# Performance work log

Hardware: AMD Instinct MI355X
Metric: run time of the kernel (lower is better)

Reference implementation:

```python
import jax, jax.numpy as jnp
import numpy as np


def setup_inputs() -> dict:
    key = jax.random.key(0)
    k1, k2, k3, k4 = jax.random.split(key, 4)
    in_features, out_features = 4096, 11008
    n_tokens = 64
    x = jax.random.normal(k1, (n_tokens, in_features), dtype=jnp.float32)
    # int8-valued weights stored as int32 (values in [-128, 127] range subset)
    weight_int = jax.random.randint(k2, (out_features, in_features), 0, 127, dtype=jnp.int32)
    weight_scale = jnp.float32(0.01)
    weight_zero_point = 3  # scalar int zero point
    bias = jax.random.normal(k3, (out_features,), dtype=jnp.float32) * 0.02
    return {
        "x": x,
        "weight_int": weight_int,
        "weight_scale": weight_scale,
        "weight_zero_point": weight_zero_point,
        "bias": bias,
    }


def reference(x, weight_int, weight_scale, weight_zero_point, bias):
    # Dequantize: W = (W_int - zp) * scale, shape [out, in]
    w = (weight_int.astype(jnp.float32) - jnp.float32(weight_zero_point)) * weight_scale
    # F.linear: y = x @ W^T + b
    out = jnp.einsum("ti,oi->to", x, w)
    return out + bias
```

## Files before the change

### kernel.cpp

```cpp
#include <hip/hip_runtime.h>
#include <hip/hip_bf16.h>

typedef __attribute__((ext_vector_type(8))) short short8;
typedef __attribute__((ext_vector_type(4))) float f32x4;
typedef __attribute__((ext_vector_type(4))) int   int4v;

#define IN_F  4096
#define OUT_F 11008
#define NTOK  64
#define BK    64
#define NIT   (IN_F / BK)
#define DEPTH 4

__device__ __forceinline__ short bf16_rne(float f) {
    unsigned u = __builtin_bit_cast(unsigned, f);
    u += 0x7FFFu + ((u >> 16) & 1u);
    return (short)(u >> 16);
}

__device__ __forceinline__ void gld16(const void* g, void* l) {
    __builtin_amdgcn_global_load_lds(
        (const __attribute__((address_space(1))) unsigned int*)g,
        (__attribute__((address_space(3))) unsigned int*)l,
        16, 0, 0);
}

__global__ __launch_bounds__(256)
void xcast(const float* __restrict__ x, unsigned short* __restrict__ xb) {
    const int i = (blockIdx.x * 256 + threadIdx.x) * 8;
    f32x4 a = *(const f32x4*)(x + i);
    f32x4 b = *(const f32x4*)(x + i + 4);
    short8 o;
#pragma unroll
    for (int j = 0; j < 4; ++j) { o[j] = bf16_rne(a[j]); o[j + 4] = bf16_rne(b[j]); }
    *(short8*)(xb + i) = o;
}

#define STAGE(IT) do {                                                        \
    const int _s = (IT) & (DEPTH - 1);                                        \
    gld16(wsrc + (size_t)(IT) * BK,             (char*)wt[_s] + tid * 16);    \
    gld16(xsrc + (size_t)(IT) * BK,             (char*)xt[_s] + tid * 16);    \
    gld16(xsrc + (size_t)(IT) * BK + 32 * IN_F, (char*)xt[_s] + tid * 16 + 4096); \
} while (0)

#define KSTEP(S, KK) do {                                                     \
    const char* _wb = (const char*)wt[S] + l15 * 256;                         \
    const char* _ab = (const char*)xt[S] + (wv * 16 + l15) * 128;             \
    const int _cw = (KK) * 8 + lg * 2;                                        \
    const int _ca = (KK) * 4 + lg;                                            \
    int4v  _b0 = *(const int4v*)(_wb + (((_cw    ) ^ rswz) * 16));            \
    int4v  _b1 = *(const int4v*)(_wb + (((_cw + 1) ^ rswz) * 16));            \
    short8 _aw = *(const short8*)(_ab + ((_ca ^ rswz) * 16));                 \
    short8 _bw;                                                               \
    _Pragma("unroll")                                                         \
    for (int j = 0; j < 4; ++j) {                                             \
        float f0 = (float)(_b0[j] - zp);                                      \
        float f1 = (float)(_b1[j] - zp);                                      \
        _bw[j]     = (short)(__builtin_bit_cast(unsigned, f0) >> 16);         \
        _bw[j + 4] = (short)(__builtin_bit_cast(unsigned, f1) >> 16);         \
    }                                                                         \
    acc = __builtin_amdgcn_mfma_f32_16x16x32_bf16(_aw, _bw, acc, 0, 0, 0);    \
} while (0)

#define WAIT_BAR(N) do {                                                      \
    asm volatile("s_waitcnt vmcnt(" #N ")" ::: "memory");                     \
    __builtin_amdgcn_s_barrier();                                             \
    asm volatile("" ::: "memory");                                            \
} while (0)

__global__ __launch_bounds__(256, 3)
void qlin3(const unsigned short* __restrict__ xb, const int* __restrict__ w,
           const float* __restrict__ scale_p, const int* __restrict__ zp_p,
           const float* __restrict__ bias, float* __restrict__ out)
{
    __shared__ __align__(16) int            wt[DEPTH][16 * BK];
    __shared__ __align__(16) unsigned short xt[DEPTH][64 * BK];

    const int tid  = threadIdx.x;
    const int lane = tid & 63;
    const int wv   = tid >> 6;
    const int l15  = lane & 15;
    const int lg   = lane >> 4;
    const int o0   = blockIdx.x * 16;

    const int   zp    = zp_p[0];
    const float scale = scale_p[0];

    const int wr = tid >> 4;
    const int wc = (tid & 15) ^ (wr & 7);
    const int* wsrc = w + (size_t)(o0 + wr) * IN_F + wc * 4;

    const int xr = tid >> 3;
    const int xc = (tid & 7) ^ (xr & 7);
    const unsigned short* xsrc = xb + (size_t)xr * IN_F + xc * 8;

    const int rswz = l15 & 7;

    f32x4 acc = {0.f, 0.f, 0.f, 0.f};

    STAGE(0);
    STAGE(1);

#pragma unroll 2
    for (int it = 0; it < NIT - 2; ++it) {
        STAGE(it + 2);
        WAIT_BAR(6);
        const int s = it & (DEPTH - 1);
        KSTEP(s, 0);
        KSTEP(s, 1);
    }
    WAIT_BAR(3);
    KSTEP((NIT - 2) & (DEPTH - 1), 0);
    KSTEP((NIT - 2) & (DEPTH - 1), 1);
    WAIT_BAR(0);
    KSTEP((NIT - 1) & (DEPTH - 1), 0);
    KSTEP((NIT - 1) & (DEPTH - 1), 1);

    {
        const int   o  = o0 + l15;
        const float bb = bias[o];
#pragma unroll
        for (int r = 0; r < 4; ++r) {
            const int t = wv * 16 + lg * 4 + r;
            out[(size_t)t * OUT_F + o] = scale * acc[r] + bb;
        }
    }
}

extern "C" void kernel_launch(void* const* d_in, const int* in_sizes, int n_in,
                              void* d_out, int out_size, void* d_ws, size_t ws_size,
                              hipStream_t stream) {
    const float* x     = (const float*)d_in[0];
    const int*   w     = (const int*)d_in[1];
    const float* scale = (const float*)d_in[2];
    const int*   zp    = (const int*)d_in[3];
    const float* bias  = (const float*)d_in[4];
    float*       out   = (float*)d_out;
    unsigned short* xbf = (unsigned short*)d_ws;

    xcast<<<dim3(128), dim3(256), 0, stream>>>(x, xbf);
    qlin3<<<dim3(OUT_F / 16), dim3(256), 0, stream>>>(xbf, w, scale, zp, bias, out);
}
```

Measured before the change: 55.45 us.

## Split K across blocks, dequantize weights once into LDS, load activations to registers

Splits the K dimension in two so there are twice as many blocks, and accumulates partial results into a bias-initialized output with atomic adds. A new bias-init kernel runs before the GEMM. Each weight tile is dequantized to bf16 once per block into a shared buffer rather than per wave, and activations are loaded straight into registers with inline asm instead of being staged through LDS. This is meant to raise occupancy and parallelism and cut redundant conversion work, at the cost of an extra launch, atomic traffic and a nondeterministic summation order.

```diff
diff --git a/kernel.cpp b/kernel.cpp
--- a/kernel.cpp
+++ b/kernel.cpp
@@ -4,13 +4,15 @@
 typedef __attribute__((ext_vector_type(8))) short short8;
 typedef __attribute__((ext_vector_type(4))) float f32x4;
 typedef __attribute__((ext_vector_type(4))) int   int4v;
+typedef __attribute__((ext_vector_type(2))) unsigned int uint2v;
 
-#define IN_F  4096
-#define OUT_F 11008
-#define NTOK  64
-#define BK    64
-#define NIT   (IN_F / BK)
-#define DEPTH 4
+#define IN_F   4096
+#define OUT_F  11008
+#define KSPLIT 2
+#define KHALF  (IN_F / KSPLIT)
+#define BK     64
+#define NIT    (KHALF / BK)
+#define WROW   72
 
 __device__ __forceinline__ short bf16_rne(float f) {
     unsigned u = __builtin_bit_cast(unsigned, f);
@@ -36,93 +38,110 @@
     *(short8*)(xb + i) = o;
 }
 
-#define STAGE(IT) do {                                                        \
-    const int _s = (IT) & (DEPTH - 1);                                        \
-    gld16(wsrc + (size_t)(IT) * BK,             (char*)wt[_s] + tid * 16);    \
-    gld16(xsrc + (size_t)(IT) * BK,             (char*)xt[_s] + tid * 16);    \
-    gld16(xsrc + (size_t)(IT) * BK + 32 * IN_F, (char*)xt[_s] + tid * 16 + 4096); \
+__global__ __launch_bounds__(256)
+void binit(const float* __restrict__ bias, float* __restrict__ out) {
+    const unsigned cid = blockIdx.x * 256 + threadIdx.x;
+    const unsigned row = cid / (OUT_F / 8);
+    const unsigned o   = (cid - row * (OUT_F / 8)) * 8;
+    f32x4 b0 = *(const f32x4*)(bias + o);
+    f32x4 b1 = *(const f32x4*)(bias + o + 4);
+    float* dst = out + (size_t)row * OUT_F + o;
+    *(f32x4*)dst = b0;
+    *(f32x4*)(dst + 4) = b1;
+}
+
+#define GLD_W(CHUNK, SLOT) gld16(wsrc + (size_t)(CHUNK) * BK, (char*)wi[SLOT] + tid * 16)
+
+#define ALOAD(D0, D1, IT) do {                                                   \
+    const int _it = ((IT) < NIT) ? (IT) : (NIT - 1);                             \
+    const char* _p = abase + (size_t)_it * 128;                                  \
+    asm volatile("global_load_dwordx4 %0, %2, off\n\t"                           \
+                 "global_load_dwordx4 %1, %2, off offset:64"                     \
+                 : "=&v"(D0), "=&v"(D1) : "v"(_p));                              \
 } while (0)
 
-#define KSTEP(S, KK) do {                                                     \
-    const char* _wb = (const char*)wt[S] + l15 * 256;                         \
-    const char* _ab = (const char*)xt[S] + (wv * 16 + l15) * 128;             \
-    const int _cw = (KK) * 8 + lg * 2;                                        \
-    const int _ca = (KK) * 4 + lg;                                            \
-    int4v  _b0 = *(const int4v*)(_wb + (((_cw    ) ^ rswz) * 16));            \
-    int4v  _b1 = *(const int4v*)(_wb + (((_cw + 1) ^ rswz) * 16));            \
-    short8 _aw = *(const short8*)(_ab + ((_ca ^ rswz) * 16));                 \
-    short8 _bw;                                                               \
-    _Pragma("unroll")                                                         \
-    for (int j = 0; j < 4; ++j) {                                             \
-        float f0 = (float)(_b0[j] - zp);                                      \
-        float f1 = (float)(_b1[j] - zp);                                      \
-        _bw[j]     = (short)(__builtin_bit_cast(unsigned, f0) >> 16);         \
-        _bw[j + 4] = (short)(__builtin_bit_cast(unsigned, f1) >> 16);         \
-    }                                                                         \
-    acc = __builtin_amdgcn_mfma_f32_16x16x32_bf16(_aw, _bw, acc, 0, 0, 0);    \
+#define DEQ(DQS, WBW) do {                                                       \
+    int4v _q = *(const int4v*)((const char*)wi[DQS] + tid * 16);                 \
+    unsigned _x0 = __builtin_bit_cast(unsigned, (float)(_q[0] - zp));            \
+    unsigned _x1 = __builtin_bit_cast(unsigned, (float)(_q[1] - zp));            \
+    unsigned _x2 = __builtin_bit_cast(unsigned, (float)(_q[2] - zp));            \
+    unsigned _x3 = __builtin_bit_cast(unsigned, (float)(_q[3] - zp));            \
+    uint2v _r;                                                                   \
+    _r[0] = (_x0 >> 16) | (_x1 & 0xffff0000u);                                   \
+    _r[1] = (_x2 >> 16) | (_x3 & 0xffff0000u);                                   \
+    *(uint2v*)&wb[WBW][dqw] = _r;                                                \
 } while (0)
 
-#define WAIT_BAR(N) do {                                                      \
-    asm volatile("s_waitcnt vmcnt(" #N ")" ::: "memory");                     \
-    __builtin_amdgcn_s_barrier();                                             \
-    asm volatile("" ::: "memory");                                            \
+#define MM(WBR, CUR) do {                                                        \
+    short8 _b0 = *(const short8*)&wb[WBR][boff];                                 \
+    short8 _b1 = *(const short8*)&wb[WBR][boff + 32];                            \
+    acc = __builtin_amdgcn_mfma_f32_16x16x32_bf16(CUR##k0, _b0, acc, 0, 0, 0);   \
+    acc = __builtin_amdgcn_mfma_f32_16x16x32_bf16(CUR##k1, _b1, acc, 0, 0, 0);   \
 } while (0)
 
-__global__ __launch_bounds__(256, 3)
-void qlin3(const unsigned short* __restrict__ xb, const int* __restrict__ w,
+#define BODY(IT, P, CUR, NX2, DQS, WBW, WBR) do {                                \
+    asm volatile("s_waitcnt vmcnt(4) lgkmcnt(0)" ::: "memory");                  \
+    __builtin_amdgcn_s_barrier();                                                \
+    __builtin_amdgcn_sched_barrier(0);                                           \
+    ALOAD(NX2##k0, NX2##k1, (IT) + 2);                                           \
+    { int _c = (IT) + 4; if (_c > NIT - 1) _c = NIT - 1; GLD_W(_c, P); }         \
+    DEQ(DQS, WBW);                                                               \
+    MM(WBR, CUR);                                                                \
+} while (0)
+
+__global__ __launch_bounds__(256, 4)
+void qlin4(const unsigned short* __restrict__ xb, const int* __restrict__ w,
            const float* __restrict__ scale_p, const int* __restrict__ zp_p,
-           const float* __restrict__ bias, float* __restrict__ out)
+           float* __restrict__ out)
 {
-    __shared__ __align__(16) int            wt[DEPTH][16 * BK];
-    __shared__ __align__(16) unsigned short xt[DEPTH][64 * BK];
+    __shared__ __align__(16) int            wi[4][16 * BK];
+    __shared__ __align__(16) unsigned short wb[2][16 * WROW];
 
     const int tid  = threadIdx.x;
     const int lane = tid & 63;
     const int wv   = tid >> 6;
     const int l15  = lane & 15;
     const int lg   = lane >> 4;
-    const int o0   = blockIdx.x * 16;
+
+    const int ob = blockIdx.x >> 1;
+    const int kh = blockIdx.x & 1;
+    const int o0 = ob * 16;
+    const int kb = kh * KHALF;
 
     const int   zp    = zp_p[0];
     const float scale = scale_p[0];
 
-    const int wr = tid >> 4;
-    const int wc = (tid & 15) ^ (wr & 7);
-    const int* wsrc = w + (size_t)(o0 + wr) * IN_F + wc * 4;
-
-    const int xr = tid >> 3;
-    const int xc = (tid & 7) ^ (xr & 7);
-    const unsigned short* xsrc = xb + (size_t)xr * IN_F + xc * 8;
-
-    const int rswz = l15 & 7;
+    const int* wsrc = w + (size_t)(o0 + (tid >> 4)) * IN_F + kb + (tid & 15) * 4;
+    const char* abase = (const char*)(xb + (size_t)(wv * 16 + l15) * IN_F + kb + lg * 8);
+    const int dqw  = (tid >> 4) * WROW + (tid & 15) * 4;
+    const int boff = l15 * WROW + lg * 8;
 
     f32x4 acc = {0.f, 0.f, 0.f, 0.f};
+    short8 A0k0, A0k1, A1k0, A1k1, A2k0, A2k1, A3k0, A3k1;
 
-    STAGE(0);
-    STAGE(1);
+    GLD_W(0, 0);
+    GLD_W(1, 1);
+    ALOAD(A0k0, A0k1, 0);
+    GLD_W(2, 2);
+    ALOAD(A1k0, A1k1, 1);
+    GLD_W(3, 3);
+    asm volatile("s_waitcnt vmcnt(7)" ::: "memory");
+    __builtin_amdgcn_s_barrier();
+    DEQ(0, 0);
 
-#pragma unroll 2
-    for (int it = 0; it < NIT - 2; ++it) {
-        STAGE(it + 2);
-        WAIT_BAR(6);
-        const int s = it & (DEPTH - 1);
-        KSTEP(s, 0);
-        KSTEP(s, 1);
+    for (int ib = 0; ib < NIT; ib += 4) {
+        BODY(ib + 0, 0, A0, A2, 1, 1, 0);
+        BODY(ib + 1, 1, A1, A3, 2, 0, 1);
+        BODY(ib + 2, 2, A2, A0, 3, 1, 0);
+        BODY(ib + 3, 3, A3, A1, 0, 0, 1);
     }
-    WAIT_BAR(3);
-    KSTEP((NIT - 2) & (DEPTH - 1), 0);
-    KSTEP((NIT - 2) & (DEPTH - 1), 1);
-    WAIT_BAR(0);
-    KSTEP((NIT - 1) & (DEPTH - 1), 0);
-    KSTEP((NIT - 1) & (DEPTH - 1), 1);
 
     {
-        const int   o  = o0 + l15;
-        const float bb = bias[o];
+        const int o = o0 + l15;
 #pragma unroll
         for (int r = 0; r < 4; ++r) {
             const int t = wv * 16 + lg * 4 + r;
-            out[(size_t)t * OUT_F + o] = scale * acc[r] + bb;
+            unsafeAtomicAdd(out + (size_t)t * OUT_F + o, scale * acc[r]);
         }
     }
 }
@@ -139,5 +158,6 @@
     unsigned short* xbf = (unsigned short*)d_ws;
 
     xcast<<<dim3(128), dim3(256), 0, stream>>>(x, xbf);
-    qlin3<<<dim3(OUT_F / 16), dim3(256), 0, stream>>>(xbf, w, scale, zp, bias, out);
+    binit<<<dim3(344), dim3(256), 0, stream>>>(bias, out);
+    qlin4<<<dim3((OUT_F / 16) * KSPLIT), dim3(256), 0, stream>>>(xbf, w, scale, zp, out);
 }
```

Result: slower. 66.04 us (+19.1%).

## Split K across two blocks with atomic accumulation and deepen prefetch pipeline

Applied to the files above, without the earlier changes.

Each output tile is now handled by two blocks, each reducing half of the input dimension. The halves are combined with float atomic adds into an output buffer that a new kernel first fills with the bias. The load pipeline now issues three stages ahead, with the barrier placed before the next stage is issued, so one barrier per iteration also protects the slot being overwritten. This doubles the grid to get more loads in flight against the bandwidth-bound weight stream. The cost is an extra launch, atomic traffic on the output, and a non-deterministic summation order.

```diff
diff --git a/kernel.cpp b/kernel.cpp
--- a/kernel.cpp
+++ b/kernel.cpp
@@ -5,12 +5,13 @@
 typedef __attribute__((ext_vector_type(4))) float f32x4;
 typedef __attribute__((ext_vector_type(4))) int   int4v;
 
-#define IN_F  4096
-#define OUT_F 11008
-#define NTOK  64
-#define BK    64
-#define NIT   (IN_F / BK)
-#define DEPTH 4
+#define IN_F   4096
+#define OUT_F  11008
+#define KSPLIT 2
+#define KHALF  (IN_F / KSPLIT)
+#define BK     64
+#define NIT    (KHALF / BK)
+#define DEPTH  4
 
 __device__ __forceinline__ short bf16_rne(float f) {
     unsigned u = __builtin_bit_cast(unsigned, f);
@@ -34,6 +35,18 @@
 #pragma unroll
     for (int j = 0; j < 4; ++j) { o[j] = bf16_rne(a[j]); o[j + 4] = bf16_rne(b[j]); }
     *(short8*)(xb + i) = o;
+}
+
+__global__ __launch_bounds__(256)
+void binit(const float* __restrict__ bias, float* __restrict__ out) {
+    const unsigned cid = blockIdx.x * 256 + threadIdx.x;
+    const unsigned row = cid / (OUT_F / 8);
+    const unsigned o   = (cid - row * (OUT_F / 8)) * 8;
+    f32x4 b0 = *(const f32x4*)(bias + o);
+    f32x4 b1 = *(const f32x4*)(bias + o + 4);
+    float* dst = out + (size_t)row * OUT_F + o;
+    *(f32x4*)dst = b0;
+    *(f32x4*)(dst + 4) = b1;
 }
 
 #define STAGE(IT) do {                                                        \
@@ -62,16 +75,10 @@
     acc = __builtin_amdgcn_mfma_f32_16x16x32_bf16(_aw, _bw, acc, 0, 0, 0);    \
 } while (0)
 
-#define WAIT_BAR(N) do {                                                      \
-    asm volatile("s_waitcnt vmcnt(" #N ")" ::: "memory");                     \
-    __builtin_amdgcn_s_barrier();                                             \
-    asm volatile("" ::: "memory");                                            \
-} while (0)
-
 __global__ __launch_bounds__(256, 3)
-void qlin3(const unsigned short* __restrict__ xb, const int* __restrict__ w,
+void qlin5(const unsigned short* __restrict__ xb, const int* __restrict__ w,
            const float* __restrict__ scale_p, const int* __restrict__ zp_p,
-           const float* __restrict__ bias, float* __restrict__ out)
+           float* __restrict__ out)
 {
     __shared__ __align__(16) int            wt[DEPTH][16 * BK];
     __shared__ __align__(16) unsigned short xt[DEPTH][64 * BK];
@@ -81,18 +88,22 @@
     const int wv   = tid >> 6;
     const int l15  = lane & 15;
     const int lg   = lane >> 4;
-    const int o0   = blockIdx.x * 16;
+
+    const int ob = blockIdx.x >> 1;
+    const int kh = blockIdx.x & 1;
+    const int o0 = ob * 16;
+    const int kb = kh * KHALF;
 
     const int   zp    = zp_p[0];
     const float scale = scale_p[0];
 
     const int wr = tid >> 4;
     const int wc = (tid & 15) ^ (wr & 7);
-    const int* wsrc = w + (size_t)(o0 + wr) * IN_F + wc * 4;
+    const int* wsrc = w + (size_t)(o0 + wr) * IN_F + kb + wc * 4;
 
     const int xr = tid >> 3;
     const int xc = (tid & 7) ^ (xr & 7);
-    const unsigned short* xsrc = xb + (size_t)xr * IN_F + xc * 8;
+    const unsigned short* xsrc = xb + (size_t)xr * IN_F + kb + xc * 8;
 
     const int rswz = l15 & 7;
 
@@ -100,29 +111,31 @@
 
     STAGE(0);
     STAGE(1);
+    STAGE(2);
 
-#pragma unroll 2
     for (int it = 0; it < NIT - 2; ++it) {
-        STAGE(it + 2);
-        WAIT_BAR(6);
+        asm volatile("s_waitcnt vmcnt(6)" ::: "memory");
+        __builtin_amdgcn_s_barrier();
+        if (it + 3 < NIT) STAGE(it + 3);
         const int s = it & (DEPTH - 1);
         KSTEP(s, 0);
         KSTEP(s, 1);
     }
-    WAIT_BAR(3);
+    asm volatile("s_waitcnt vmcnt(3)" ::: "memory");
+    __builtin_amdgcn_s_barrier();
     KSTEP((NIT - 2) & (DEPTH - 1), 0);
     KSTEP((NIT - 2) & (DEPTH - 1), 1);
-    WAIT_BAR(0);
+    asm volatile("s_waitcnt vmcnt(0)" ::: "memory");
+    __builtin_amdgcn_s_barrier();
     KSTEP((NIT - 1) & (DEPTH - 1), 0);
     KSTEP((NIT - 1) & (DEPTH - 1), 1);
 
     {
-        const int   o  = o0 + l15;
-        const float bb = bias[o];
+        const int o = o0 + l15;
 #pragma unroll
         for (int r = 0; r < 4; ++r) {
             const int t = wv * 16 + lg * 4 + r;
-            out[(size_t)t * OUT_F + o] = scale * acc[r] + bb;
+            unsafeAtomicAdd(out + (size_t)t * OUT_F + o, scale * acc[r]);
         }
     }
 }
@@ -139,5 +152,6 @@
     unsigned short* xbf = (unsigned short*)d_ws;
 
     xcast<<<dim3(128), dim3(256), 0, stream>>>(x, xbf);
-    qlin3<<<dim3(OUT_F / 16), dim3(256), 0, stream>>>(xbf, w, scale, zp, bias, out);
+    binit<<<dim3(344), dim3(256), 0, stream>>>(bias, out);
+    qlin5<<<dim3((OUT_F / 16) * KSPLIT), dim3(256), 0, stream>>>(xbf, w, scale, zp, out);
 }
```

Result: no change. 56.02 us (+1.0%).
